# Optimization experiments

Measured on AMD Instinct MI355X. Metric: run time of the kernel, lower is better.

The kernel has to match this reference:

```python
import jax, jax.numpy as jnp
import numpy as np
import math

GOLDEN_CENTER = 1.0 / math.e
GOLDEN_LOWER = 0.5 - math.log(4.0 / 3.0)
GOLDEN_UPPER = 0.5

B, T, D = 4, 2048, 1024
E = 8
I = 4096 // (E // 2)  # expert_inter = 1024


def setup_inputs() -> dict:
    key = jax.random.key(0)
    k = jax.random.split(key, 6)
    s_d = 1.0 / math.sqrt(D)
    s_i = 1.0 / math.sqrt(I)
    return {
        "x": jax.random.normal(k[0], (B, T, D), jnp.float32),
        "Wg": jax.random.normal(k[1], (E, D, I), jnp.float32) * s_d,
        "Wu": jax.random.normal(k[2], (E, D, I), jnp.float32) * s_d,
        "Wd": jax.random.normal(k[3], (E, I, D), jnp.float32) * s_i,
        "Wr": jax.random.normal(k[4], (D, E), jnp.float32) * s_d,
        "temperature": jnp.ones((1,), jnp.float32),
    }


def _routing_weights(x, Wr, temperature):
    # inhibition: [B,T,E]
    inh = jax.nn.sigmoid((x @ Wr) / temperature)
    in_zone = (inh >= GOLDEN_LOWER) & (inh <= GOLDEN_UPPER)
    dist = jnp.abs(inh - GOLDEN_CENTER)
    w = jnp.exp(-dist / 0.1) * in_zone.astype(x.dtype)
    wsum = w.sum(axis=-1, keepdims=True)
    no_expert = wsum < 1e-8
    # fallback: softer decay, keep top-2 experts, renormalize
    fb = jnp.exp(-dist / 0.3)
    _, top2 = jax.lax.top_k(fb, 2)  # [B,T,2]
    fb_mask = jax.nn.one_hot(top2, E, dtype=x.dtype).sum(axis=-2)  # [B,T,E]
    fb_w = fb * fb_mask
    fb_w = fb_w / jnp.clip(fb_w.sum(axis=-1, keepdims=True), 1e-8)
    w = jnp.where(no_expert, fb_w, w)
    wsum = w.sum(axis=-1, keepdims=True)
    return w / jnp.clip(wsum, 1e-8)


def reference(x, Wg, Wu, Wd, Wr, temperature):
    weights = _routing_weights(x, Wr, temperature)  # [B,T,E]
    gate = jnp.einsum("btd,edi->beti", x, Wg)
    up = jnp.einsum("btd,edi->beti", x, Wu)
    h = jax.nn.silu(gate) * up  # [B,E,T,I]
    e_out = jnp.einsum("beti,eid->betd", h, Wd)
    out = jnp.einsum("bte,betd->btd", weights, e_out)
    return out
```

## Files before the change

kernel.cpp:

```cpp
#include <hip/hip_runtime.h>
#include <hip/hip_bf16.h>
#include <cstdint>

typedef __attribute__((ext_vector_type(8))) _Float16 f16x8;
typedef __attribute__((ext_vector_type(4))) _Float16 f16x4;
typedef __attribute__((ext_vector_type(4))) float f32x4;

#define GOLDEN_CENTER_F 0.36787944117144233f
#define GOLDEN_LOWER_F  0.21231792754821915f
#define GOLDEN_UPPER_F  0.5f

static constexpr int Dm = 1024;
static constexpr int Im = 1024;
static constexpr int NTOK = 8192;
static constexpr int NE = 8;

__device__ __forceinline__ void async16(const _Float16* g, _Float16* l) {
  __builtin_amdgcn_global_load_lds(
      (const __attribute__((address_space(1))) void*)g,
      (__attribute__((address_space(3))) void*)l,
      16, 0, 0);
}

__global__ void routing_kernel(const float* __restrict__ x, const float* __restrict__ Wr,
                               const float* __restrict__ temp, float* __restrict__ wts) {
  const int wave = threadIdx.x >> 6, lane = threadIdx.x & 63;
  const int t = blockIdx.x * 4 + wave;
  const float* xr = x + (size_t)t * Dm;
  float acc[NE] = {0.f,0.f,0.f,0.f,0.f,0.f,0.f,0.f};
  for (int d = lane; d < Dm; d += 64) {
    float xv = xr[d];
    const float* wr = Wr + (size_t)d * NE;
#pragma unroll
    for (int e = 0; e < NE; ++e) acc[e] += xv * wr[e];
  }
#pragma unroll
  for (int off = 32; off > 0; off >>= 1) {
#pragma unroll
    for (int e = 0; e < NE; ++e) acc[e] += __shfl_down(acc[e], off, 64);
  }
  if (lane == 0) {
    float T = temp[0];
    float w[NE], dist[NE];
    float wsum = 0.f;
#pragma unroll
    for (int e = 0; e < NE; ++e) {
      float inh = 1.f / (1.f + expf(-acc[e] / T));
      dist[e] = fabsf(inh - GOLDEN_CENTER_F);
      bool zone = (inh >= GOLDEN_LOWER_F) && (inh <= GOLDEN_UPPER_F);
      w[e] = zone ? expf(-dist[e] / 0.1f) : 0.f;
      wsum += w[e];
    }
    if (wsum < 1e-8f) {
      float fb[NE];
#pragma unroll
      for (int e = 0; e < NE; ++e) fb[e] = expf(-dist[e] / 0.3f);
      int i1 = 0;
      for (int e = 1; e < NE; ++e) if (fb[e] > fb[i1]) i1 = e;
      int i2 = (i1 == 0) ? 1 : 0;
      for (int e = 0; e < NE; ++e) if (e != i1 && fb[e] > fb[i2]) i2 = e;
      float s = fmaxf(fb[i1] + fb[i2], 1e-8f);
#pragma unroll
      for (int e = 0; e < NE; ++e) w[e] = 0.f;
      w[i1] = fb[i1] / s;
      w[i2] = fb[i2] / s;
      wsum = w[i1] + w[i2];
    }
    float inv = 1.f / fmaxf(wsum, 1e-8f);
#pragma unroll
    for (int e = 0; e < NE; ++e) wts[(size_t)t * NE + e] = w[e] * inv;
  }
}

__global__ void compact_kernel(const float* __restrict__ wts, int* __restrict__ tok,
                               float* __restrict__ wc, int* __restrict__ cnt) {
  const int e = blockIdx.x;
  const int tid = threadIdx.x;
  const int wave = tid >> 6, lane = tid & 63;
  __shared__ int wcnt[4];
  __shared__ int s_running;
  if (tid == 0) s_running = 0;
  __syncthreads();
  for (int base = 0; base < NTOK; base += 256) {
    int t = base + tid;
    float w = wts[(size_t)t * NE + e];
    bool act = w > 0.f;
    unsigned long long mask = __ballot(act);
    int prefix = __popcll(mask & ((1ull << lane) - 1ull));
    if (lane == 0) wcnt[wave] = __popcll(mask);
    __syncthreads();
    int wbase = 0;
    for (int i = 0; i < wave; ++i) wbase += wcnt[i];
    int run = s_running;
    if (act) {
      int pos = run + wbase + prefix;
      tok[(size_t)e * NTOK + pos] = t;
      wc[(size_t)e * NTOK + pos] = w;
    }
    __syncthreads();
    if (tid == 0) s_running = run + wcnt[0] + wcnt[1] + wcnt[2] + wcnt[3];
    __syncthreads();
  }
  int c = s_running;
  if (tid == 0) cnt[e] = c;
  int padded = (c + 127) & ~127;
  for (int p = c + tid; p < padded; p += 256) {
    tok[(size_t)e * NTOK + p] = 0;
    wc[(size_t)e * NTOK + p] = 0.f;
  }
}

__global__ void cvt_x_kernel(const float* __restrict__ x, _Float16* __restrict__ xb) {
  size_t i = ((size_t)blockIdx.x * 256 + threadIdx.x) * 4;
  float4 v = *(const float4*)(x + i);
  f16x4 o = {(_Float16)v.x, (_Float16)v.y, (_Float16)v.z, (_Float16)v.w};
  *(f16x4*)(xb + i) = o;
}

__global__ void zero_kernel(float4* __restrict__ p) {
  p[(size_t)blockIdx.x * 256 + threadIdx.x] = float4{0.f, 0.f, 0.f, 0.f};
}

__global__ void transpose_cvt_kernel(const float* __restrict__ Wg, const float* __restrict__ Wu,
                                     const float* __restrict__ Wd, _Float16* __restrict__ WgT,
                                     _Float16* __restrict__ WuT, _Float16* __restrict__ WdT) {
  __shared__ float tile[32][33];
  const int which = blockIdx.z >> 3;
  const int e = blockIdx.z & 7;
  const float* src = which == 0 ? Wg : which == 1 ? Wu : Wd;
  _Float16* dst = which == 0 ? WgT : which == 1 ? WuT : WdT;
  const size_t base = (size_t)e * 1024 * 1024;
  const int r0 = blockIdx.y * 32, c0 = blockIdx.x * 32;
  const int tx = threadIdx.x & 31, ty = threadIdx.x >> 5;
#pragma unroll
  for (int j = 0; j < 32; j += 8)
    tile[ty + j][tx] = src[base + (size_t)(r0 + ty + j) * 1024 + c0 + tx];
  __syncthreads();
#pragma unroll
  for (int j = 0; j < 32; j += 8)
    dst[base + (size_t)(c0 + ty + j) * 1024 + r0 + tx] = (_Float16)tile[tx][ty + j];
}

__global__ __launch_bounds__(256, 2) void gemm1_kernel(
    const _Float16* __restrict__ A, const _Float16* __restrict__ BgAll,
    const _Float16* __restrict__ BuAll, const int* __restrict__ tok,
    const int* __restrict__ cnt, _Float16* __restrict__ hbuf) {
  constexpr int K = Dm;
  const int e = blockIdx.z;
  const int r0 = blockIdx.y * 128;
  if (r0 >= cnt[e]) return;
  const int n0 = blockIdx.x * 128;
  const _Float16* Bg = BgAll + (size_t)e * Dm * Im;
  const _Float16* Bu = BuAll + (size_t)e * Dm * Im;
  _Float16* H = hbuf + (size_t)e * NTOK * Im;
  const int* tk = tok + (size_t)e * NTOK;

  __shared__ _Float16 As[128 * 32];
  __shared__ _Float16 Bgs[128 * 32];
  __shared__ _Float16 Bus[128 * 32];
  const int tid = threadIdx.x;
  const int wave = tid >> 6, lane = tid & 63;
  const int m_off = (wave & 1) * 64, n_off = (wave >> 1) * 64;

  f32x4 accg[4][4], accu[4][4];
#pragma unroll
  for (int i = 0; i < 4; ++i)
#pragma unroll
    for (int j = 0; j < 4; ++j) { accg[i][j] = (f32x4)0.f; accu[i][j] = (f32x4)0.f; }

  const int srow = lane >> 2;
  const int scol = (lane & 3) * 8;
  const int ridx = r0 + wave * 32 + srow;
  const int tA0 = tk[ridx];
  const int tA1 = tk[ridx + 16];
  const _Float16* gA0 = A + (size_t)tA0 * K + scol;
  const _Float16* gA1 = A + (size_t)tA1 * K + scol;
  const _Float16* gBg = Bg + (size_t)(n0 + wave * 32 + srow) * K + scol;
  const _Float16* gBu = Bu + (size_t)(n0 + wave * 32 + srow) * K + scol;
  _Float16* lA  = As  + (wave * 32) * 32;
  _Float16* lBg = Bgs + (wave * 32) * 32;
  _Float16* lBu = Bus + (wave * 32) * 32;

  const int fr = lane & 15, fq = lane >> 4;
  const int aoff = (m_off + fr) * 32 + fq * 8;
  const int boff = (n_off + fr) * 32 + fq * 8;

  for (int k0 = 0; k0 < K; k0 += 32) {
    __syncthreads();
    async16(gA0 + k0, lA);
    async16(gA1 + k0, lA + 16 * 32);
    async16(gBg + k0, lBg);
    async16(gBg + k0 + 16 * K, lBg + 16 * 32);
    async16(gBu + k0, lBu);
    async16(gBu + k0 + 16 * K, lBu + 16 * 32);
    __syncthreads();

    f16x8 af[4], bgf[4], buf2[4];
#pragma unroll
    for (int i = 0; i < 4; ++i) {
      af[i]   = *(const f16x8*)(As  + aoff + i * 16 * 32);
      bgf[i]  = *(const f16x8*)(Bgs + boff + i * 16 * 32);
      buf2[i] = *(const f16x8*)(Bus + boff + i * 16 * 32);
    }
#pragma unroll
    for (int im = 0; im < 4; ++im)
#pragma unroll
      for (int in2 = 0; in2 < 4; ++in2) {
        accg[im][in2] = __builtin_amdgcn_mfma_f32_16x16x32_f16(af[im], bgf[in2], accg[im][in2], 0, 0, 0);
        accu[im][in2] = __builtin_amdgcn_mfma_f32_16x16x32_f16(af[im], buf2[in2], accu[im][in2], 0, 0, 0);
      }
  }

#pragma unroll
  for (int im = 0; im < 4; ++im)
#pragma unroll
    for (int in2 = 0; in2 < 4; ++in2)
#pragma unroll
      for (int r = 0; r < 4; ++r) {
        int row = r0 + m_off + im * 16 + fq * 4 + r;
        int c = n0 + n_off + in2 * 16 + fr;
        float g = accg[im][in2][r], u = accu[im][in2][r];
        float s = g / (1.f + __expf(-g));
        H[(size_t)row * Im + c] = (_Float16)(s * u);
      }
}

__global__ __launch_bounds__(256, 2) void gemm2_kernel(
    const _Float16* __restrict__ hbuf, const _Float16* __restrict__ BAll,
    const int* __restrict__ tok, const float* __restrict__ wc,
    const int* __restrict__ cnt, float* __restrict__ out) {
  constexpr int K = Im;
  const int e = blockIdx.z;
  const int r0 = blockIdx.y * 128;
  if (r0 >= cnt[e]) return;
  const int n0 = blockIdx.x * 128;
  const _Float16* A = hbuf + (size_t)e * NTOK * Im;
  const _Float16* B = BAll + (size_t)e * Im * Dm;

  __shared__ _Float16 As[128 * 32];
  __shared__ _Float16 Bs[128 * 32];
  __shared__ float wloc[128];
  __shared__ int tloc[128];
  const int tid = threadIdx.x;
  const int wave = tid >> 6, lane = tid & 63;
  const int m_off = (wave & 1) * 64, n_off = (wave >> 1) * 64;

  if (tid < 128) {
    wloc[tid] = wc[(size_t)e * NTOK + r0 + tid];
    tloc[tid] = tok[(size_t)e * NTOK + r0 + tid];
  }

  f32x4 acc[4][4];
#pragma unroll
  for (int i = 0; i < 4; ++i)
#pragma unroll
    for (int j = 0; j < 4; ++j) acc[i][j] = (f32x4)0.f;

  const int srow = lane >> 2;
  const int scol = (lane & 3) * 8;
  const _Float16* gA = A + (size_t)(r0 + wave * 32 + srow) * K + scol;
  const _Float16* gB = B + (size_t)(n0 + wave * 32 + srow) * K + scol;
  _Float16* lA = As + (wave * 32) * 32;
  _Float16* lB = Bs + (wave * 32) * 32;

  const int fr = lane & 15, fq = lane >> 4;
  const int aoff = (m_off + fr) * 32 + fq * 8;
  const int boff = (n_off + fr) * 32 + fq * 8;

  for (int k0 = 0; k0 < K; k0 += 32) {
    __syncthreads();
    async16(gA + k0, lA);
    async16(gA + k0 + 16 * K, lA + 16 * 32);
    async16(gB + k0, lB);
    async16(gB + k0 + 16 * K, lB + 16 * 32);
    __syncthreads();

    f16x8 af[4], bf[4];
#pragma unroll
    for (int i = 0; i < 4; ++i) {
      af[i] = *(const f16x8*)(As + aoff + i * 16 * 32);
      bf[i] = *(const f16x8*)(Bs + boff + i * 16 * 32);
    }
#pragma unroll
    for (int im = 0; im < 4; ++im)
#pragma unroll
      for (int in2 = 0; in2 < 4; ++in2)
        acc[im][in2] = __builtin_amdgcn_mfma_f32_16x16x32_f16(af[im], bf[in2], acc[im][in2], 0, 0, 0);
  }
  __syncthreads();

#pragma unroll
  for (int im = 0; im < 4; ++im)
#pragma unroll
    for (int in2 = 0; in2 < 4; ++in2)
#pragma unroll
      for (int r = 0; r < 4; ++r) {
        int row = m_off + im * 16 + fq * 4 + r;
        int t = tloc[row];
        float wv = wloc[row];
        int c = n0 + n_off + in2 * 16 + fr;
        atomicAdd(out + (size_t)t * Dm + c, acc[im][in2][r] * wv);
      }
}

extern "C" void kernel_launch(void* const* d_in, const int* in_sizes, int n_in,
                              void* d_out, int out_size, void* d_ws, size_t ws_size,
                              hipStream_t stream) {
  const float* x    = (const float*)d_in[0];
  const float* Wg   = (const float*)d_in[1];
  const float* Wu   = (const float*)d_in[2];
  const float* Wd   = (const float*)d_in[3];
  const float* Wr   = (const float*)d_in[4];
  const float* temp = (const float*)d_in[5];
  float* out = (float*)d_out;

  char* ws = (char*)d_ws;
  float* wts = (float*)ws;
  int*   tok = (int*)(ws + (1 << 18));
  float* wc  = (float*)(ws + 2 * (1 << 18));
  int*   cnt = (int*)(ws + 3 * (1 << 18));
  _Float16* xb  = (_Float16*)(ws + 3 * (1 << 18) + 4096);
  _Float16* WgT = xb  + (size_t)NTOK * Dm;
  _Float16* WuT = WgT + (size_t)NE * Dm * Im;
  _Float16* WdT = WuT + (size_t)NE * Dm * Im;
  _Float16* hbuf = WdT + (size_t)NE * Dm * Im;

  routing_kernel<<<NTOK / 4, 256, 0, stream>>>(x, Wr, temp, wts);
  compact_kernel<<<NE, 256, 0, stream>>>(wts, tok, wc, cnt);
  cvt_x_kernel<<<(NTOK * Dm) / 1024, 256, 0, stream>>>(x, xb);
  transpose_cvt_kernel<<<dim3(32, 32, 24), 256, 0, stream>>>(Wg, Wu, Wd, WgT, WuT, WdT);
  zero_kernel<<<(NTOK * Dm / 4) / 256, 256, 0, stream>>>((float4*)out);

  gemm1_kernel<<<dim3(Im / 128, NTOK / 128, NE), 256, 0, stream>>>(xb, WgT, WuT, tok, cnt, hbuf);
  gemm2_kernel<<<dim3(Dm / 128, NTOK / 128, NE), 256, 0, stream>>>(hbuf, WdT, tok, wc, cnt, out);
}
```

Baseline: 569.7 us.

## Replace atomic scatter-add with per-expert fp16 output buffer and gather combine

gemm2 now writes each expert's output rows as fp16 into a dense per-expert buffer instead of doing fp32 atomicAdd scatter into out. A new combine kernel gathers, for each token, the rows of its active experts through a position map built by compaction, weights them and writes out. This removes the zero kernel and the atomic traffic. In exchange it adds an extra round trip through memory, fp16 rounding of expert outputs, and an expert-group loop that is chosen from the workspace size.

```diff
diff --git a/kernel.cpp b/kernel.cpp
--- a/kernel.cpp
+++ b/kernel.cpp
@@ -73,7 +73,8 @@
 }
 
 __global__ void compact_kernel(const float* __restrict__ wts, int* __restrict__ tok,
-                               float* __restrict__ wc, int* __restrict__ cnt) {
+                               float* __restrict__ wc, int* __restrict__ cnt,
+                               int* __restrict__ pos) {
   const int e = blockIdx.x;
   const int tid = threadIdx.x;
   const int wave = tid >> 6, lane = tid & 63;
@@ -92,10 +93,11 @@
     int wbase = 0;
     for (int i = 0; i < wave; ++i) wbase += wcnt[i];
     int run = s_running;
+    int p = run + wbase + prefix;
+    pos[(size_t)t * NE + e] = act ? p : -1;
     if (act) {
-      int pos = run + wbase + prefix;
-      tok[(size_t)e * NTOK + pos] = t;
-      wc[(size_t)e * NTOK + pos] = w;
+      tok[(size_t)e * NTOK + p] = t;
+      wc[(size_t)e * NTOK + p] = w;
     }
     __syncthreads();
     if (tid == 0) s_running = run + wcnt[0] + wcnt[1] + wcnt[2] + wcnt[3];
@@ -115,10 +117,6 @@
   float4 v = *(const float4*)(x + i);
   f16x4 o = {(_Float16)v.x, (_Float16)v.y, (_Float16)v.z, (_Float16)v.w};
   *(f16x4*)(xb + i) = o;
-}
-
-__global__ void zero_kernel(float4* __restrict__ p) {
-  p[(size_t)blockIdx.x * 256 + threadIdx.x] = float4{0.f, 0.f, 0.f, 0.f};
 }
 
 __global__ void transpose_cvt_kernel(const float* __restrict__ Wg, const float* __restrict__ Wu,
@@ -144,15 +142,16 @@
 __global__ __launch_bounds__(256, 2) void gemm1_kernel(
     const _Float16* __restrict__ A, const _Float16* __restrict__ BgAll,
     const _Float16* __restrict__ BuAll, const int* __restrict__ tok,
-    const int* __restrict__ cnt, _Float16* __restrict__ hbuf) {
+    const int* __restrict__ cnt, _Float16* __restrict__ hbuf, int ebase) {
   constexpr int K = Dm;
-  const int e = blockIdx.z;
+  const int z = blockIdx.z;
+  const int e = ebase + z;
   const int r0 = blockIdx.y * 128;
   if (r0 >= cnt[e]) return;
   const int n0 = blockIdx.x * 128;
   const _Float16* Bg = BgAll + (size_t)e * Dm * Im;
   const _Float16* Bu = BuAll + (size_t)e * Dm * Im;
-  _Float16* H = hbuf + (size_t)e * NTOK * Im;
+  _Float16* H = hbuf + (size_t)z * NTOK * Im;
   const int* tk = tok + (size_t)e * NTOK;
 
   __shared__ _Float16 As[128 * 32];
@@ -227,28 +226,22 @@
 
 __global__ __launch_bounds__(256, 2) void gemm2_kernel(
     const _Float16* __restrict__ hbuf, const _Float16* __restrict__ BAll,
-    const int* __restrict__ tok, const float* __restrict__ wc,
-    const int* __restrict__ cnt, float* __restrict__ out) {
+    const int* __restrict__ cnt, _Float16* __restrict__ ebuf, int ebase) {
   constexpr int K = Im;
-  const int e = blockIdx.z;
+  const int z = blockIdx.z;
+  const int e = ebase + z;
   const int r0 = blockIdx.y * 128;
   if (r0 >= cnt[e]) return;
   const int n0 = blockIdx.x * 128;
-  const _Float16* A = hbuf + (size_t)e * NTOK * Im;
+  const _Float16* A = hbuf + (size_t)z * NTOK * Im;
   const _Float16* B = BAll + (size_t)e * Im * Dm;
+  _Float16* Ez = ebuf + (size_t)z * NTOK * Dm;
 
   __shared__ _Float16 As[128 * 32];
   __shared__ _Float16 Bs[128 * 32];
-  __shared__ float wloc[128];
-  __shared__ int tloc[128];
   const int tid = threadIdx.x;
   const int wave = tid >> 6, lane = tid & 63;
   const int m_off = (wave & 1) * 64, n_off = (wave >> 1) * 64;
-
-  if (tid < 128) {
-    wloc[tid] = wc[(size_t)e * NTOK + r0 + tid];
-    tloc[tid] = tok[(size_t)e * NTOK + r0 + tid];
-  }
 
   f32x4 acc[4][4];
 #pragma unroll
@@ -287,7 +280,6 @@
       for (int in2 = 0; in2 < 4; ++in2)
         acc[im][in2] = __builtin_amdgcn_mfma_f32_16x16x32_f16(af[im], bf[in2], acc[im][in2], 0, 0, 0);
   }
-  __syncthreads();
 
 #pragma unroll
   for (int im = 0; im < 4; ++im)
@@ -296,11 +288,38 @@
 #pragma unroll
       for (int r = 0; r < 4; ++r) {
         int row = m_off + im * 16 + fq * 4 + r;
-        int t = tloc[row];
-        float wv = wloc[row];
         int c = n0 + n_off + in2 * 16 + fr;
-        atomicAdd(out + (size_t)t * Dm + c, acc[im][in2][r] * wv);
+        Ez[((size_t)(r0 + row)) * Dm + c] = (_Float16)acc[im][in2][r];
       }
+}
+
+__global__ void combine_kernel(const _Float16* __restrict__ ebuf, const int* __restrict__ pos,
+                               const float* __restrict__ wts, float* __restrict__ out,
+                               int ebase, int g, int accum) {
+  const int t = blockIdx.x;
+  __shared__ int sp[NE];
+  __shared__ float sw[NE];
+  if (threadIdx.x < g) {
+    sp[threadIdx.x] = pos[(size_t)t * NE + ebase + threadIdx.x];
+    sw[threadIdx.x] = wts[(size_t)t * NE + ebase + threadIdx.x];
+  }
+  __syncthreads();
+  const int c = threadIdx.x * 4;
+  float4 s;
+  if (accum) s = *(const float4*)(out + (size_t)t * Dm + c);
+  else s = float4{0.f, 0.f, 0.f, 0.f};
+  for (int j = 0; j < g; ++j) {
+    int p = sp[j];
+    if (p >= 0) {
+      float w = sw[j];
+      f16x4 v = *(const f16x4*)(ebuf + ((size_t)j * NTOK + p) * Dm + c);
+      s.x += w * (float)v[0];
+      s.y += w * (float)v[1];
+      s.z += w * (float)v[2];
+      s.w += w * (float)v[3];
+    }
+  }
+  *(float4*)(out + (size_t)t * Dm + c) = s;
 }
 
 extern "C" void kernel_launch(void* const* d_in, const int* in_sizes, int n_in,
@@ -315,22 +334,35 @@
   float* out = (float*)d_out;
 
   char* ws = (char*)d_ws;
-  float* wts = (float*)ws;
-  int*   tok = (int*)(ws + (1 << 18));
-  float* wc  = (float*)(ws + 2 * (1 << 18));
-  int*   cnt = (int*)(ws + 3 * (1 << 18));
-  _Float16* xb  = (_Float16*)(ws + 3 * (1 << 18) + 4096);
-  _Float16* WgT = xb  + (size_t)NTOK * Dm;
-  _Float16* WuT = WgT + (size_t)NE * Dm * Im;
-  _Float16* WdT = WuT + (size_t)NE * Dm * Im;
-  _Float16* hbuf = WdT + (size_t)NE * Dm * Im;
+  size_t off = 0;
+  auto carve = [&](size_t bytes) {
+    char* p = ws + off;
+    off = (off + bytes + 255) & ~(size_t)255;
+    return p;
+  };
+  float* wts = (float*)carve((size_t)NTOK * NE * 4);
+  int*   tok = (int*)  carve((size_t)NE * NTOK * 4);
+  float* wc  = (float*)carve((size_t)NE * NTOK * 4);
+  int*   pos = (int*)  carve((size_t)NTOK * NE * 4);
+  int*   cnt = (int*)  carve(4096);
+  _Float16* xb   = (_Float16*)carve((size_t)NTOK * Dm * 2);
+  _Float16* WgT  = (_Float16*)carve((size_t)NE * Dm * Im * 2);
+  _Float16* WuT  = (_Float16*)carve((size_t)NE * Dm * Im * 2);
+  _Float16* WdT  = (_Float16*)carve((size_t)NE * Dm * Im * 2);
+  const size_t fixed_off = off;
+  const size_t per_expert = (size_t)NTOK * Im * 2 + (size_t)NTOK * Dm * 2;
+  int g = (ws_size >= fixed_off + 8 * per_expert) ? 8 : 4;
+  _Float16* hbuf = (_Float16*)carve((size_t)g * NTOK * Im * 2);
+  _Float16* ebuf = (_Float16*)carve((size_t)g * NTOK * Dm * 2);
 
   routing_kernel<<<NTOK / 4, 256, 0, stream>>>(x, Wr, temp, wts);
-  compact_kernel<<<NE, 256, 0, stream>>>(wts, tok, wc, cnt);
+  compact_kernel<<<NE, 256, 0, stream>>>(wts, tok, wc, cnt, pos);
   cvt_x_kernel<<<(NTOK * Dm) / 1024, 256, 0, stream>>>(x, xb);
   transpose_cvt_kernel<<<dim3(32, 32, 24), 256, 0, stream>>>(Wg, Wu, Wd, WgT, WuT, WdT);
-  zero_kernel<<<(NTOK * Dm / 4) / 256, 256, 0, stream>>>((float4*)out);
-
-  gemm1_kernel<<<dim3(Im / 128, NTOK / 128, NE), 256, 0, stream>>>(xb, WgT, WuT, tok, cnt, hbuf);
-  gemm2_kernel<<<dim3(Dm / 128, NTOK / 128, NE), 256, 0, stream>>>(hbuf, WdT, tok, wc, cnt, out);
-}
+
+  for (int e0 = 0; e0 < NE; e0 += g) {
+    gemm1_kernel<<<dim3(Im / 128, NTOK / 128, g), 256, 0, stream>>>(xb, WgT, WuT, tok, cnt, hbuf, e0);
+    gemm2_kernel<<<dim3(Dm / 128, NTOK / 128, g), 256, 0, stream>>>(hbuf, WdT, cnt, ebuf, e0);
+    combine_kernel<<<NTOK, 256, 0, stream>>>(ebuf, pos, wts, out, e0, g, e0 > 0);
+  }
+}
```

Measured after the change: 486.7 us. 14.6% less time.
